# Performance work log

Hardware: AMD Instinct MI355X
Metric: run time of the kernel (lower is better)

Reference implementation:

```python
import jax, jax.numpy as jnp
import numpy as np

D_MODEL = 1024
D_INNER = 2048   # d_model * expansion_factor(2)
D_CONV = 4
N_EXPERTS = 8
TOP_K = 2


def setup_inputs() -> dict:
    key = jax.random.key(0)
    ks = jax.random.split(key, 6)
    s = 0.02
    return {
        "x": jax.random.normal(ks[0], (4, 2048, D_MODEL), jnp.float32),
        "Wr": jax.random.normal(ks[1], (N_EXPERTS, D_MODEL), jnp.float32) * s,
        "br": jnp.zeros((N_EXPERTS,), jnp.float32),
        "Win": jax.random.normal(ks[2], (N_EXPERTS, 2 * D_INNER, D_MODEL), jnp.float32) * s,
        "conv_w": jax.random.normal(ks[3], (N_EXPERTS, D_INNER, D_CONV), jnp.float32) * s,
        "conv_b": jnp.zeros((N_EXPERTS, D_INNER), jnp.float32),
        "Dp": jnp.ones((N_EXPERTS, D_INNER), jnp.float32),
        "Wout": jax.random.normal(ks[4], (N_EXPERTS, D_MODEL, D_INNER), jnp.float32) * s,
    }


def reference(x, Wr, br, Win, conv_w, conv_b, Dp, Wout):
    B, L, C = x.shape
    xf = x.reshape(-1, C)                                   # [N, C]
    logits = xf @ Wr.T + br                                 # [N, E]
    probs = jax.nn.softmax(logits.astype(jnp.float32), axis=-1)
    tw, ti = jax.lax.top_k(probs, TOP_K)                    # [N, k]
    tw = tw / jnp.sum(tw, axis=-1, keepdims=True)
    oh = jax.nn.one_hot(ti, N_EXPERTS, dtype=jnp.float32)   # [N, k, E]
    load = oh.sum(1).mean(0)                                # [E]
    aux_loss = jnp.sum(load * load)
    # per-token combine weight for each expert (sum over top-k slots)
    cw = jnp.einsum('nk,nke->ne', tw, oh)                   # [N, E]
    out = jnp.zeros_like(xf)
    for j in range(N_EXPERTS):
        # Per-token expert (L=1 inside the original loop): causal depthwise
        # conv with left padding reduces to last-tap * x + bias.
        xz = xf @ Win[j].T                                  # [N, 2*D_INNER]
        xi, z = xz[:, :D_INNER], xz[:, D_INNER:]
        xa = jax.nn.silu(xi * conv_w[j, :, -1] + conv_b[j])
        y = xa * Dp[j] * jax.nn.silu(z)
        out = out + cw[:, j:j + 1].astype(xf.dtype) * (y @ Wout[j].T)
    return out.reshape(B, L, C), aux_loss
```

## Files before the change

### kernel.cpp

```cpp
#include <hip/hip_runtime.h>
#include <hip/hip_bf16.h>
#include <stdint.h>

#define NTOK 8192
#define CDIM 1024
#define DIN  2048
#define NEXP 8
#define NSLOT (NTOK * 2)

typedef __bf16 bf16x8 __attribute__((ext_vector_type(8)));
typedef float  f32x4  __attribute__((ext_vector_type(4)));

typedef __attribute__((address_space(1))) const unsigned char GBUF;
typedef __attribute__((address_space(3))) unsigned char LBUF;

__device__ __forceinline__ void gload_lds16(const void* g, void* l) {
    __builtin_amdgcn_global_load_lds((GBUF*)g, (LBUF*)l, 16, 0, 0);
}

__device__ __forceinline__ ushort f2bf(float f) {
    union { float f; unsigned u; } v; v.f = f;
    unsigned u = v.u;
    u += 0x7fffu + ((u >> 16) & 1u);
    return (ushort)(u >> 16);
}
__device__ __forceinline__ float bf2f(ushort u) {
    union { float f; unsigned u; } v; v.u = ((unsigned)u) << 16; return v.f;
}
__device__ __forceinline__ float silu_f(float x) { return x / (1.f + __expf(-x)); }

__device__ __forceinline__ bf16x8 lds_swz(const ushort* L, int row, int kof) {
    return *(const bf16x8*)&L[row * 64 + ((((kof >> 3) ^ row) & 7) << 3)];
}

#define WAITV(N) asm volatile("s_waitcnt vmcnt(" #N ")" ::: "memory")
#define BARR     __builtin_amdgcn_s_barrier()

__global__ void __launch_bounds__(256) k_cvt(const float* __restrict__ src,
                                             ushort* __restrict__ dst, int n4) {
    int i = blockIdx.x * 256 + threadIdx.x;
    int stride = gridDim.x * 256;
    for (; i < n4; i += stride) {
        float4 v = ((const float4*)src)[i];
        ushort4 o;
        o.x = f2bf(v.x); o.y = f2bf(v.y); o.z = f2bf(v.z); o.w = f2bf(v.w);
        ((ushort4*)dst)[i] = o;
    }
}

__global__ void __launch_bounds__(256) k_router(
    const float* __restrict__ x, const float* __restrict__ Wr,
    const float* __restrict__ br, int* __restrict__ counts,
    int* __restrict__ tok_e, float* __restrict__ tok_w,
    ushort* __restrict__ xb) {
    int wave = blockIdx.x * 4 + (threadIdx.x >> 6);
    int lane = threadIdx.x & 63;
    const float4* row = (const float4*)(x + (size_t)wave * CDIM);
    ushort4* xrow = (ushort4*)(xb + (size_t)wave * CDIM);
    float acc[NEXP];
#pragma unroll
    for (int e = 0; e < NEXP; ++e) acc[e] = 0.f;
#pragma unroll
    for (int j = 0; j < 4; ++j) {
        float4 v = row[j * 64 + lane];
        ushort4 o;
        o.x = f2bf(v.x); o.y = f2bf(v.y); o.z = f2bf(v.z); o.w = f2bf(v.w);
        xrow[j * 64 + lane] = o;
#pragma unroll
        for (int e = 0; e < NEXP; ++e) {
            float4 w = ((const float4*)(Wr + e * CDIM))[j * 64 + lane];
            acc[e] += v.x * w.x + v.y * w.y + v.z * w.z + v.w * w.w;
        }
    }
#pragma unroll
    for (int off = 32; off > 0; off >>= 1)
#pragma unroll
        for (int e = 0; e < NEXP; ++e) acc[e] += __shfl_xor(acc[e], off, 64);
    if (lane == 0) {
        float l[NEXP];
#pragma unroll
        for (int e = 0; e < NEXP; ++e) l[e] = acc[e] + br[e];
        int i0 = 0; float l0 = l[0];
#pragma unroll
        for (int e = 1; e < NEXP; ++e) if (l[e] > l0) { l0 = l[e]; i0 = e; }
        int i1 = -1; float l1 = -1e30f;
#pragma unroll
        for (int e = 0; e < NEXP; ++e) if (e != i0 && l[e] > l1) { l1 = l[e]; i1 = e; }
        float s  = __expf(l1 - l0);
        float w0 = 1.f / (1.f + s);
        float w1 = 1.f - w0;
        tok_e[wave * 2] = i0; tok_e[wave * 2 + 1] = i1;
        tok_w[wave * 2] = w0; tok_w[wave * 2 + 1] = w1;
        atomicAdd(&counts[i0], 1); atomicAdd(&counts[i1], 1);
    }
}

__global__ void k_scan(const int* __restrict__ counts, int* __restrict__ offsets,
                       float* __restrict__ out_aux) {
    if (threadIdx.x == 0 && blockIdx.x == 0) {
        int o = 0;
        for (int e = 0; e < NEXP; ++e) { offsets[e] = o; o += counts[e]; }
        offsets[NEXP] = o;
        float aux = 0.f;
        for (int e = 0; e < NEXP; ++e) {
            float ld = (float)counts[e] * (1.f / (float)NTOK);
            aux += ld * ld;
        }
        *out_aux = aux;
    }
}

__global__ void __launch_bounds__(256) k_scatter(
    const int* __restrict__ tok_e, const float* __restrict__ tok_w,
    const int* __restrict__ offsets, int* __restrict__ cursor,
    int* __restrict__ perm_token, int* __restrict__ tok_slot) {
    int t = blockIdx.x * 256 + threadIdx.x;
    if (t >= NTOK) return;
#pragma unroll
    for (int k = 0; k < 2; ++k) {
        int e = tok_e[t * 2 + k];
        int pos = atomicAdd(&cursor[e], 1);
        int s = offsets[e] + pos;
        perm_token[s] = t;
        tok_slot[t * 2 + k] = s;
    }
}

__global__ void __launch_bounds__(512, 2) k_gemm1(
    const ushort* __restrict__ xb, const ushort* __restrict__ Winb,
    const float* __restrict__ conv_w, const float* __restrict__ conv_b,
    const float* __restrict__ Dp, const int* __restrict__ counts,
    const int* __restrict__ offsets, const int* __restrict__ perm_token,
    ushort* __restrict__ y) {
    int h = blockIdx.x;
    int vb = (h & 7) * 160 + (h >> 3);
    int e   = vb / 160;
    int r   = vb % 160;
    int mt0 = r >> 4;
    int nt  = r & 15;
    int cnt = counts[e];
    if (cnt == 0) return;
    int base = offsets[e];
    int mtiles = (cnt + 255) >> 8;
    int n0 = nt * 128;

    __shared__ ushort aL[2][256 * 64];
    __shared__ ushort bL[2][256 * 64];

    int tid = threadIdx.x, lane = tid & 63, w = tid >> 6;
    int Mw = w >> 1, Nw = w & 1;
    const ushort* WinE = Winb + (size_t)e * (2 * DIN) * CDIM;
    int schunk = ((tid & 7) ^ ((tid >> 3) & 7)) << 3;

    uint bsrc[4];
#pragma unroll
    for (int i = 0; i < 4; ++i) {
        int rr = i * 64 + (tid >> 3);
        int grow = (rr < 128) ? (n0 + rr) : (DIN + n0 + (rr - 128));
        bsrc[i] = (uint)grow * CDIM + schunk;
    }

    for (int mt = mt0; mt < mtiles; mt += 10) {
        int rem = cnt - mt * 256;
        uint asrc[4];
#pragma unroll
        for (int i = 0; i < 4; ++i) {
            int rr = i * 64 + (tid >> 3);
            int sidx = base + mt * 256 + (rr < rem ? rr : 0);
            asrc[i] = (uint)perm_token[sidx] * CDIM + schunk;
        }

        f32x4 accXi[4][4], accZ[4][4];
#pragma unroll
        for (int m = 0; m < 4; ++m)
#pragma unroll
            for (int n = 0; n < 4; ++n) {
                accXi[m][n] = f32x4{0.f, 0.f, 0.f, 0.f};
                accZ[m][n]  = f32x4{0.f, 0.f, 0.f, 0.f};
            }

        auto stgA = [&](int bi, int ko, int i, int j) {
            gload_lds16(xb + asrc[i] + ko, &aL[bi][(i * 512 + tid) * 8]);
            gload_lds16(xb + asrc[j] + ko, &aL[bi][(j * 512 + tid) * 8]);
        };
        auto stgB = [&](int bi, int ko, int i, int j) {
            gload_lds16(WinE + bsrc[i] + ko, &bL[bi][(i * 512 + tid) * 8]);
            gload_lds16(WinE + bsrc[j] + ko, &bL[bi][(j * 512 + tid) * 8]);
        };

        bf16x8 af0[4], af1[4], bx[4], bz[4];
        stgA(0, 0, 0, 1); stgA(0, 0, 2, 3); stgB(0, 0, 0, 1); stgB(0, 0, 2, 3);

#pragma unroll 1
        for (int kt = 0; kt < 16; ++kt) {
            int cur = kt & 1, nxt = cur ^ 1;
            const ushort* A = aL[cur];
            const ushort* B = bL[cur];
            int ko = (kt + 1) * 64;
            bool st = kt < 15;
            WAITV(2);
            BARR;
#pragma unroll
            for (int m = 0; m < 4; ++m)
                af0[m] = lds_swz(A, Mw * 64 + m * 16 + (lane & 15), (lane >> 4) * 8);
#pragma unroll
            for (int n = 0; n < 4; ++n)
                bx[n] = lds_swz(B, Nw * 64 + n * 16 + (lane & 15), (lane >> 4) * 8);
            if (st) stgA(nxt, ko, 0, 1);
            __builtin_amdgcn_s_setprio(1);
#pragma unroll
            for (int m = 0; m < 4; ++m)
#pragma unroll
                for (int n = 0; n < 4; ++n)
                    accXi[m][n] = __builtin_amdgcn_mfma_f32_16x16x32_bf16(af0[m], bx[n], accXi[m][n], 0, 0, 0);
            __builtin_amdgcn_s_setprio(0);
            if (st) { WAITV(2); } else { WAITV(0); }
            BARR;
#pragma unroll
            for (int n = 0; n < 4; ++n)
                bz[n] = lds_swz(B, 128 + Nw * 64 + n * 16 + (lane & 15), (lane >> 4) * 8);
            if (st) stgA(nxt, ko, 2, 3);
            __builtin_amdgcn_s_setprio(1);
#pragma unroll
            for (int m = 0; m < 4; ++m)
#pragma unroll
                for (int n = 0; n < 4; ++n)
                    accZ[m][n] = __builtin_amdgcn_mfma_f32_16x16x32_bf16(af0[m], bz[n], accZ[m][n], 0, 0, 0);
            __builtin_amdgcn_s_setprio(0);
            BARR;
#pragma unroll
            for (int m = 0; m < 4; ++m)
                af1[m] = lds_swz(A, Mw * 64 + m * 16 + (lane & 15), 32 + (lane >> 4) * 8);
#pragma unroll
            for (int n = 0; n < 4; ++n)
                bx[n] = lds_swz(B, Nw * 64 + n * 16 + (lane & 15), 32 + (lane >> 4) * 8);
            if (st) stgB(nxt, ko, 0, 1);
            __builtin_amdgcn_s_setprio(1);
#pragma unroll
            for (int m = 0; m < 4; ++m)
#pragma unroll
                for (int n = 0; n < 4; ++n)
                    accXi[m][n] = __builtin_amdgcn_mfma_f32_16x16x32_bf16(af1[m], bx[n], accXi[m][n], 0, 0, 0);
            __builtin_amdgcn_s_setprio(0);
            BARR;
#pragma unroll
            for (int n = 0; n < 4; ++n)
                bz[n] = lds_swz(B, 128 + Nw * 64 + n * 16 + (lane & 15), 32 + (lane >> 4) * 8);
            if (st) stgB(nxt, ko, 2, 3);
            __builtin_amdgcn_s_setprio(1);
#pragma unroll
            for (int m = 0; m < 4; ++m)
#pragma unroll
                for (int n = 0; n < 4; ++n)
                    accZ[m][n] = __builtin_amdgcn_mfma_f32_16x16x32_bf16(af1[m], bz[n], accZ[m][n], 0, 0, 0);
            __builtin_amdgcn_s_setprio(0);
        }
        __syncthreads();

#pragma unroll
        for (int n = 0; n < 4; ++n) {
            int c = n0 + Nw * 64 + n * 16 + (lane & 15);
            float cwl = conv_w[((size_t)e * DIN + c) * 4 + 3];
            float cb  = conv_b[(size_t)e * DIN + c];
            float dp  = Dp[(size_t)e * DIN + c];
#pragma unroll
            for (int m = 0; m < 4; ++m)
#pragma unroll
                for (int q = 0; q < 4; ++q) {
                    int rl = Mw * 64 + m * 16 + (lane >> 4) * 4 + q;
                    if (rl < rem) {
                        int slot = base + mt * 256 + rl;
                        float xi = accXi[m][n][q], z = accZ[m][n][q];
                        float yv = silu_f(xi * cwl + cb) * dp * silu_f(z);
                        y[(size_t)slot * DIN + c] = f2bf(yv);
                    }
                }
        }
        __syncthreads();
    }
}

__global__ void __launch_bounds__(512, 2) k_gemm2(
    const ushort* __restrict__ y, const ushort* __restrict__ Woutb,
    const int* __restrict__ counts, const int* __restrict__ offsets,
    ushort* __restrict__ so) {
    int h = blockIdx.x;
    int vb = (h & 7) * 32 + (h >> 3);
    int e   = vb >> 5;
    int r   = vb & 31;
    int nt  = r >> 3;
    int sp  = r & 7;
    int cnt = counts[e];
    if (cnt == 0) return;
    int base = offsets[e];
    int mtiles = (cnt + 255) >> 8;
    int c0 = nt * 256;

    __shared__ ushort aL[2][256 * 64];
    __shared__ ushort bL[2][256 * 64];

    int tid = threadIdx.x, lane = tid & 63, w = tid >> 6;
    int Mw = w >> 2, Nw = w & 3;
    const ushort* WoutE = Woutb + (size_t)e * CDIM * DIN;
    int schunk = ((tid & 7) ^ ((tid >> 3) & 7)) << 3;

    uint bsrc[4];
#pragma unroll
    for (int i = 0; i < 4; ++i) {
        int rr = i * 64 + (tid >> 3);
        bsrc[i] = (uint)(c0 + rr) * DIN + schunk;
    }

    for (int mt = sp; mt < mtiles; mt += 8) {
        int rem = cnt - mt * 256;
        uint asrc[4];
#pragma unroll
        for (int i = 0; i < 4; ++i) {
            int rr = i * 64 + (tid >> 3);
            int slot = base + mt * 256 + (rr < rem ? rr : 0);
            asrc[i] = (uint)slot * DIN + schunk;
        }
        f32x4 acc[8][4];
#pragma unroll
        for (int m = 0; m < 8; ++m)
#pragma unroll
            for (int n = 0; n < 4; ++n) acc[m][n] = f32x4{0.f, 0.f, 0.f, 0.f};

        auto stgA = [&](int bi, int ko, int i, int j) {
            gload_lds16(y + asrc[i] + ko, &aL[bi][(i * 512 + tid) * 8]);
            gload_lds16(y + asrc[j] + ko, &aL[bi][(j * 512 + tid) * 8]);
        };
        auto stgB = [&](int bi, int ko, int i, int j) {
            gload_lds16(WoutE + bsrc[i] + ko, &bL[bi][(i * 512 + tid) * 8]);
            gload_lds16(WoutE + bsrc[j] + ko, &bL[bi][(j * 512 + tid) * 8]);
        };

        bf16x8 afA[4], afB[4], bf0[4], bf1[4];
        stgA(0, 0, 0, 1); stgA(0, 0, 2, 3); stgB(0, 0, 0, 1); stgB(0, 0, 2, 3);

#pragma unroll 1
        for (int kt = 0; kt < 32; ++kt) {
            int cur = kt & 1, nxt = cur ^ 1;
            const ushort* A = aL[cur];
            const ushort* B = bL[cur];
            int ko = (kt + 1) * 64;
            bool st = kt < 31;
            WAITV(0);
            BARR;
#pragma unroll
            for (int m = 0; m < 4; ++m)
                afA[m] = lds_swz(A, Mw * 128 + m * 16 + (lane & 15), (lane >> 4) * 8);
#pragma unroll
            for (int n = 0; n < 4; ++n)
                bf0[n] = lds_swz(B, Nw * 64 + n * 16 + (lane & 15), (lane >> 4) * 8);
            if (st) stgA(nxt, ko, 0, 1);
            __builtin_amdgcn_s_setprio(1);
#pragma unroll
            for (int m = 0; m < 4; ++m)
#pragma unroll
                for (int n = 0; n < 4; ++n)
                    acc[m][n] = __builtin_amdgcn_mfma_f32_16x16x32_bf16(afA[m], bf0[n], acc[m][n], 0, 0, 0);
            __builtin_amdgcn_s_setprio(0);
            BARR;
#pragma unroll
            for (int m = 0; m < 4; ++m)
                afB[m] = lds_swz(A, Mw * 128 + 64 + m * 16 + (lane & 15), (lane >> 4) * 8);
            if (st) stgA(nxt, ko, 2, 3);
            __builtin_amdgcn_s_setprio(1);
#pragma unroll
            for (int m = 0; m < 4; ++m)
#pragma unroll
                for (int n = 0; n < 4; ++n)
                    acc[4 + m][n] = __builtin_amdgcn_mfma_f32_16x16x32_bf16(afB[m], bf0[n], acc[4 + m][n], 0, 0, 0);
            __builtin_amdgcn_s_setprio(0);
            BARR;
#pragma unroll
            for (int m = 0; m < 4; ++m)
                afA[m] = lds_swz(A, Mw * 128 + m * 16 + (lane & 15), 32 + (lane >> 4) * 8);
#pragma unroll
            for (int n = 0; n < 4; ++n)
                bf1[n] = lds_swz(B, Nw * 64 + n * 16 + (lane & 15), 32 + (lane >> 4) * 8);
            if (st) stgB(nxt, ko, 0, 1);
            __builtin_amdgcn_s_setprio(1);
#pragma unroll
            for (int m = 0; m < 4; ++m)
#pragma unroll
                for (int n = 0; n < 4; ++n)
                    acc[m][n] = __builtin_amdgcn_mfma_f32_16x16x32_bf16(afA[m], bf1[n], acc[m][n], 0, 0, 0);
            __builtin_amdgcn_s_setprio(0);
            BARR;
#pragma unroll
            for (int m = 0; m < 4; ++m)
                afB[m] = lds_swz(A, Mw * 128 + 64 + m * 16 + (lane & 15), 32 + (lane >> 4) * 8);
            if (st) stgB(nxt, ko, 2, 3);
            __builtin_amdgcn_s_setprio(1);
#pragma unroll
            for (int m = 0; m < 4; ++m)
#pragma unroll
                for (int n = 0; n < 4; ++n)
                    acc[4 + m][n] = __builtin_amdgcn_mfma_f32_16x16x32_bf16(afB[m], bf1[n], acc[4 + m][n], 0, 0, 0);
            __builtin_amdgcn_s_setprio(0);
        }
        __syncthreads();

#pragma unroll
        for (int m = 0; m < 8; ++m)
#pragma unroll
            for (int q = 0; q < 4; ++q) {
                int rl = Mw * 128 + m * 16 + (lane >> 4) * 4 + q;
                if (rl < rem) {
                    int slot = base + mt * 256 + rl;
#pragma unroll
                    for (int n = 0; n < 4; ++n) {
                        int col = c0 + Nw * 64 + n * 16 + (lane & 15);
                        so[(size_t)slot * CDIM + col] = f2bf(acc[m][n][q]);
                    }
                }
            }
        __syncthreads();
    }
}

__global__ void __launch_bounds__(256) k_combine(
    const ushort* __restrict__ so, const int* __restrict__ tok_slot,
    const float* __restrict__ tok_w, float* __restrict__ out) {
    int i = blockIdx.x * 256 + threadIdx.x;
    int t  = i >> 7;
    int c8 = (i & 127) << 3;
    int s0 = tok_slot[t * 2], s1 = tok_slot[t * 2 + 1];
    float w0 = tok_w[t * 2],  w1 = tok_w[t * 2 + 1];
    uint4 a = *(const uint4*)(so + (size_t)s0 * CDIM + c8);
    uint4 b = *(const uint4*)(so + (size_t)s1 * CDIM + c8);
    const ushort* au = (const ushort*)&a;
    const ushort* bu = (const ushort*)&b;
    float4 o0, o1;
    o0.x = w0 * bf2f(au[0]) + w1 * bf2f(bu[0]);
    o0.y = w0 * bf2f(au[1]) + w1 * bf2f(bu[1]);
    o0.z = w0 * bf2f(au[2]) + w1 * bf2f(bu[2]);
    o0.w = w0 * bf2f(au[3]) + w1 * bf2f(bu[3]);
    o1.x = w0 * bf2f(au[4]) + w1 * bf2f(bu[4]);
    o1.y = w0 * bf2f(au[5]) + w1 * bf2f(bu[5]);
    o1.z = w0 * bf2f(au[6]) + w1 * bf2f(bu[6]);
    o1.w = w0 * bf2f(au[7]) + w1 * bf2f(bu[7]);
    float4* dst = (float4*)(out + (size_t)t * CDIM + c8);
    dst[0] = o0; dst[1] = o1;
}

extern "C" void kernel_launch(void* const* d_in, const int* in_sizes, int n_in,
                              void* d_out, int out_size, void* d_ws, size_t ws_size,
                              hipStream_t stream) {
    const float* x      = (const float*)d_in[0];
    const float* Wr     = (const float*)d_in[1];
    const float* br     = (const float*)d_in[2];
    const float* Win    = (const float*)d_in[3];
    const float* conv_w = (const float*)d_in[4];
    const float* conv_b = (const float*)d_in[5];
    const float* Dp     = (const float*)d_in[6];
    const float* Wout   = (const float*)d_in[7];
    float* out = (float*)d_out;

    char* ws = (char*)d_ws;
    int*    counts     = (int*)(ws + 0);
    int*    offsets    = (int*)(ws + 64);
    int*    cursor     = (int*)(ws + 128);
    int*    tok_e      = (int*)(ws + 4096);
    float*  tok_w      = (float*)(ws + 4096 + 1 * 65536);
    int*    perm_token = (int*)(ws + 4096 + 2 * 65536);
    int*    tok_slot   = (int*)(ws + 4096 + 3 * 65536);
    const size_t MB = 1u << 20;
    ushort* y     = (ushort*)(ws + MB);
    ushort* xb    = (ushort*)(ws + MB + 67108864);
    ushort* winb  = (ushort*)(ws + MB + 67108864 + 16777216);
    ushort* woutb = (ushort*)(ws + MB + 67108864 + 16777216 + 67108864);
    ushort* so    = winb;

    hipMemsetAsync(ws, 0, 256, stream);

    k_cvt<<<2048, 256, 0, stream>>>(Win,  winb,  NEXP * 2 * DIN * CDIM / 4);
    k_cvt<<<1024, 256, 0, stream>>>(Wout, woutb, NEXP * CDIM * DIN / 4);

    k_router<<<NTOK / 4, 256, 0, stream>>>(x, Wr, br, counts, tok_e, tok_w, xb);
    k_scan<<<1, 64, 0, stream>>>(counts, offsets, out + (size_t)NTOK * CDIM);
    k_scatter<<<NTOK / 256, 256, 0, stream>>>(tok_e, tok_w, offsets, cursor, perm_token, tok_slot);

    k_gemm1<<<NEXP * 160, 512, 0, stream>>>(xb, winb, conv_w, conv_b, Dp,
                                            counts, offsets, perm_token, y);
    k_gemm2<<<NEXP * 32, 512, 0, stream>>>(y, woutb, counts, offsets, so);
    k_combine<<<NTOK * 128 / 256, 256, 0, stream>>>(so, tok_slot, tok_w, out);
}
```

Measured before the change: 626.3 us.

## Flatten gemm2 into global tile list with smaller tiles and fuse weight conversions

The scan now computes per-expert tile prefix offsets, and gemm2 switches from a fixed 8-expert by 32-block grid to a flat persistent loop over all (expert, m-tile, n-tile) work items. Tiles shrink to 256x128 with a single LDS buffer and a simple load/sync/compute loop, and launch bounds rise to allow more resident blocks. This is meant to fix load imbalance across experts and under-filled CUs. The cost is losing the double-buffered, prefetch-interleaved pipeline, so global loads are no longer overlapped with MFMA within a block. The two fp32-to-bf16 weight conversion launches are also merged into one kernel.

```diff
diff --git a/kernel.cpp b/kernel.cpp
--- a/kernel.cpp
+++ b/kernel.cpp
@@ -36,15 +36,20 @@
 #define WAITV(N) asm volatile("s_waitcnt vmcnt(" #N ")" ::: "memory")
 #define BARR     __builtin_amdgcn_s_barrier()
 
-__global__ void __launch_bounds__(256) k_cvt(const float* __restrict__ src,
-                                             ushort* __restrict__ dst, int n4) {
+__global__ void __launch_bounds__(256) k_cvt2(
+    const float* __restrict__ srcA, ushort* __restrict__ dstA, int nA4,
+    const float* __restrict__ srcB, ushort* __restrict__ dstB, int nB4) {
     int i = blockIdx.x * 256 + threadIdx.x;
     int stride = gridDim.x * 256;
-    for (; i < n4; i += stride) {
-        float4 v = ((const float4*)src)[i];
+    int ntot = nA4 + nB4;
+    for (; i < ntot; i += stride) {
+        const float4* s; ushort4* d; int j;
+        if (i < nA4) { s = (const float4*)srcA; d = (ushort4*)dstA; j = i; }
+        else         { s = (const float4*)srcB; d = (ushort4*)dstB; j = i - nA4; }
+        float4 v = s[j];
         ushort4 o;
         o.x = f2bf(v.x); o.y = f2bf(v.y); o.z = f2bf(v.z); o.w = f2bf(v.w);
-        ((ushort4*)dst)[i] = o;
+        d[j] = o;
     }
 }
 
@@ -96,11 +101,17 @@
 }
 
 __global__ void k_scan(const int* __restrict__ counts, int* __restrict__ offsets,
-                       float* __restrict__ out_aux) {
+                       int* __restrict__ tileoff, float* __restrict__ out_aux) {
     if (threadIdx.x == 0 && blockIdx.x == 0) {
-        int o = 0;
-        for (int e = 0; e < NEXP; ++e) { offsets[e] = o; o += counts[e]; }
+        int o = 0, tp = 0;
+        for (int e = 0; e < NEXP; ++e) {
+            offsets[e] = o;
+            tileoff[e] = tp;
+            o += counts[e];
+            tp += (counts[e] + 255) >> 8;
+        }
         offsets[NEXP] = o;
+        tileoff[NEXP] = tp;
         float aux = 0.f;
         for (int e = 0; e < NEXP; ++e) {
             float ld = (float)counts[e] * (1.f / (float)NTOK);
@@ -280,134 +291,87 @@
     }
 }
 
-__global__ void __launch_bounds__(512, 2) k_gemm2(
+__global__ void __launch_bounds__(512, 6) k_gemm2(
     const ushort* __restrict__ y, const ushort* __restrict__ Woutb,
     const int* __restrict__ counts, const int* __restrict__ offsets,
-    ushort* __restrict__ so) {
-    int h = blockIdx.x;
-    int vb = (h & 7) * 32 + (h >> 3);
-    int e   = vb >> 5;
-    int r   = vb & 31;
-    int nt  = r >> 3;
-    int sp  = r & 7;
-    int cnt = counts[e];
-    if (cnt == 0) return;
-    int base = offsets[e];
-    int mtiles = (cnt + 255) >> 8;
-    int c0 = nt * 256;
-
-    __shared__ ushort aL[2][256 * 64];
-    __shared__ ushort bL[2][256 * 64];
+    const int* __restrict__ tileoff, ushort* __restrict__ so) {
+    __shared__ ushort aL[256 * 64];
+    __shared__ ushort bL[128 * 64];
 
     int tid = threadIdx.x, lane = tid & 63, w = tid >> 6;
-    int Mw = w >> 2, Nw = w & 3;
-    const ushort* WoutE = Woutb + (size_t)e * CDIM * DIN;
+    int Mw = w >> 1, Nw = w & 1;
     int schunk = ((tid & 7) ^ ((tid >> 3) & 7)) << 3;
 
-    uint bsrc[4];
-#pragma unroll
-    for (int i = 0; i < 4; ++i) {
-        int rr = i * 64 + (tid >> 3);
-        bsrc[i] = (uint)(c0 + rr) * DIN + schunk;
-    }
-
-    for (int mt = sp; mt < mtiles; mt += 8) {
+    int ntiles = tileoff[NEXP] * 8;
+    int b = blockIdx.x;
+    int virt = (b & 7) * 96 + (b >> 3);
+
+    for (int t = virt; t < ntiles; t += 768) {
+        int pair = t >> 3, nt = t & 7;
+        int e = 0;
+#pragma unroll
+        for (int k = 1; k < NEXP; ++k) if (pair >= tileoff[k]) e = k;
+        int mt = pair - tileoff[e];
+        int cnt = counts[e], base = offsets[e];
         int rem = cnt - mt * 256;
-        uint asrc[4];
+        int c0 = nt * 128;
+        const ushort* WoutE = Woutb + (size_t)e * CDIM * DIN;
+
+        uint asrc[4], bsrc[2];
 #pragma unroll
         for (int i = 0; i < 4; ++i) {
             int rr = i * 64 + (tid >> 3);
             int slot = base + mt * 256 + (rr < rem ? rr : 0);
             asrc[i] = (uint)slot * DIN + schunk;
         }
-        f32x4 acc[8][4];
-#pragma unroll
-        for (int m = 0; m < 8; ++m)
+#pragma unroll
+        for (int i = 0; i < 2; ++i) {
+            int rr = i * 64 + (tid >> 3);
+            bsrc[i] = (uint)(c0 + rr) * DIN + schunk;
+        }
+
+        f32x4 acc[4][4];
+#pragma unroll
+        for (int m = 0; m < 4; ++m)
 #pragma unroll
             for (int n = 0; n < 4; ++n) acc[m][n] = f32x4{0.f, 0.f, 0.f, 0.f};
-
-        auto stgA = [&](int bi, int ko, int i, int j) {
-            gload_lds16(y + asrc[i] + ko, &aL[bi][(i * 512 + tid) * 8]);
-            gload_lds16(y + asrc[j] + ko, &aL[bi][(j * 512 + tid) * 8]);
-        };
-        auto stgB = [&](int bi, int ko, int i, int j) {
-            gload_lds16(WoutE + bsrc[i] + ko, &bL[bi][(i * 512 + tid) * 8]);
-            gload_lds16(WoutE + bsrc[j] + ko, &bL[bi][(j * 512 + tid) * 8]);
-        };
-
-        bf16x8 afA[4], afB[4], bf0[4], bf1[4];
-        stgA(0, 0, 0, 1); stgA(0, 0, 2, 3); stgB(0, 0, 0, 1); stgB(0, 0, 2, 3);
 
 #pragma unroll 1
         for (int kt = 0; kt < 32; ++kt) {
-            int cur = kt & 1, nxt = cur ^ 1;
-            const ushort* A = aL[cur];
-            const ushort* B = bL[cur];
-            int ko = (kt + 1) * 64;
-            bool st = kt < 31;
-            WAITV(0);
-            BARR;
-#pragma unroll
-            for (int m = 0; m < 4; ++m)
-                afA[m] = lds_swz(A, Mw * 128 + m * 16 + (lane & 15), (lane >> 4) * 8);
-#pragma unroll
-            for (int n = 0; n < 4; ++n)
-                bf0[n] = lds_swz(B, Nw * 64 + n * 16 + (lane & 15), (lane >> 4) * 8);
-            if (st) stgA(nxt, ko, 0, 1);
-            __builtin_amdgcn_s_setprio(1);
-#pragma unroll
-            for (int m = 0; m < 4; ++m)
+            int ko = kt * 64;
+            gload_lds16(y + asrc[0] + ko, &aL[(0 * 512 + tid) * 8]);
+            gload_lds16(y + asrc[1] + ko, &aL[(1 * 512 + tid) * 8]);
+            gload_lds16(y + asrc[2] + ko, &aL[(2 * 512 + tid) * 8]);
+            gload_lds16(y + asrc[3] + ko, &aL[(3 * 512 + tid) * 8]);
+            gload_lds16(WoutE + bsrc[0] + ko, &bL[(0 * 512 + tid) * 8]);
+            gload_lds16(WoutE + bsrc[1] + ko, &bL[(1 * 512 + tid) * 8]);
+            __syncthreads();
+#pragma unroll
+            for (int kk = 0; kk < 64; kk += 32) {
+                int kof = kk + (lane >> 4) * 8;
+                bf16x8 af[4], bf[4];
+#pragma unroll
+                for (int m = 0; m < 4; ++m)
+                    af[m] = lds_swz(aL, Mw * 64 + m * 16 + (lane & 15), kof);
 #pragma unroll
                 for (int n = 0; n < 4; ++n)
-                    acc[m][n] = __builtin_amdgcn_mfma_f32_16x16x32_bf16(afA[m], bf0[n], acc[m][n], 0, 0, 0);
-            __builtin_amdgcn_s_setprio(0);
-            BARR;
-#pragma unroll
-            for (int m = 0; m < 4; ++m)
-                afB[m] = lds_swz(A, Mw * 128 + 64 + m * 16 + (lane & 15), (lane >> 4) * 8);
-            if (st) stgA(nxt, ko, 2, 3);
-            __builtin_amdgcn_s_setprio(1);
-#pragma unroll
-            for (int m = 0; m < 4; ++m)
-#pragma unroll
-                for (int n = 0; n < 4; ++n)
-                    acc[4 + m][n] = __builtin_amdgcn_mfma_f32_16x16x32_bf16(afB[m], bf0[n], acc[4 + m][n], 0, 0, 0);
-            __builtin_amdgcn_s_setprio(0);
-            BARR;
-#pragma unroll
-            for (int m = 0; m < 4; ++m)
-                afA[m] = lds_swz(A, Mw * 128 + m * 16 + (lane & 15), 32 + (lane >> 4) * 8);
-#pragma unroll
-            for (int n = 0; n < 4; ++n)
-                bf1[n] = lds_swz(B, Nw * 64 + n * 16 + (lane & 15), 32 + (lane >> 4) * 8);
-            if (st) stgB(nxt, ko, 0, 1);
-            __builtin_amdgcn_s_setprio(1);
-#pragma unroll
-            for (int m = 0; m < 4; ++m)
-#pragma unroll
-                for (int n = 0; n < 4; ++n)
-                    acc[m][n] = __builtin_amdgcn_mfma_f32_16x16x32_bf16(afA[m], bf1[n], acc[m][n], 0, 0, 0);
-            __builtin_amdgcn_s_setprio(0);
-            BARR;
-#pragma unroll
-            for (int m = 0; m < 4; ++m)
-                afB[m] = lds_swz(A, Mw * 128 + 64 + m * 16 + (lane & 15), 32 + (lane >> 4) * 8);
-            if (st) stgB(nxt, ko, 2, 3);
-            __builtin_amdgcn_s_setprio(1);
-#pragma unroll
-            for (int m = 0; m < 4; ++m)
-#pragma unroll
-                for (int n = 0; n < 4; ++n)
-                    acc[4 + m][n] = __builtin_amdgcn_mfma_f32_16x16x32_bf16(afB[m], bf1[n], acc[4 + m][n], 0, 0, 0);
-            __builtin_amdgcn_s_setprio(0);
-        }
-        __syncthreads();
-
-#pragma unroll
-        for (int m = 0; m < 8; ++m)
+                    bf[n] = lds_swz(bL, Nw * 64 + n * 16 + (lane & 15), kof);
+                __builtin_amdgcn_s_setprio(1);
+#pragma unroll
+                for (int m = 0; m < 4; ++m)
+#pragma unroll
+                    for (int n = 0; n < 4; ++n)
+                        acc[m][n] = __builtin_amdgcn_mfma_f32_16x16x32_bf16(af[m], bf[n], acc[m][n], 0, 0, 0);
+                __builtin_amdgcn_s_setprio(0);
+            }
+            __syncthreads();
+        }
+
+#pragma unroll
+        for (int m = 0; m < 4; ++m)
 #pragma unroll
             for (int q = 0; q < 4; ++q) {
-                int rl = Mw * 128 + m * 16 + (lane >> 4) * 4 + q;
+                int rl = Mw * 64 + m * 16 + (lane >> 4) * 4 + q;
                 if (rl < rem) {
                     int slot = base + mt * 256 + rl;
 #pragma unroll
@@ -417,7 +381,6 @@
                     }
                 }
             }
-        __syncthreads();
     }
 }
 
@@ -463,6 +426,7 @@
     int*    counts     = (int*)(ws + 0);
     int*    offsets    = (int*)(ws + 64);
     int*    cursor     = (int*)(ws + 128);
+    int*    tileoff    = (int*)(ws + 192);
     int*    tok_e      = (int*)(ws + 4096);
     float*  tok_w      = (float*)(ws + 4096 + 1 * 65536);
     int*    perm_token = (int*)(ws + 4096 + 2 * 65536);
@@ -476,15 +440,15 @@
 
     hipMemsetAsync(ws, 0, 256, stream);
 
-    k_cvt<<<2048, 256, 0, stream>>>(Win,  winb,  NEXP * 2 * DIN * CDIM / 4);
-    k_cvt<<<1024, 256, 0, stream>>>(Wout, woutb, NEXP * CDIM * DIN / 4);
+    k_cvt2<<<3072, 256, 0, stream>>>(Win,  winb,  NEXP * 2 * DIN * CDIM / 4,
+                                     Wout, woutb, NEXP * CDIM * DIN / 4);
 
     k_router<<<NTOK / 4, 256, 0, stream>>>(x, Wr, br, counts, tok_e, tok_w, xb);
-    k_scan<<<1, 64, 0, stream>>>(counts, offsets, out + (size_t)NTOK * CDIM);
+    k_scan<<<1, 64, 0, stream>>>(counts, offsets, tileoff, out + (size_t)NTOK * CDIM);
     k_scatter<<<NTOK / 256, 256, 0, stream>>>(tok_e, tok_w, offsets, cursor, perm_token, tok_slot);
 
     k_gemm1<<<NEXP * 160, 512, 0, stream>>>(xb, winb, conv_w, conv_b, Dp,
                                             counts, offsets, perm_token, y);
-    k_gemm2<<<NEXP * 32, 512, 0, stream>>>(y, woutb, counts, offsets, so);
+    k_gemm2<<<768, 512, 0, stream>>>(y, woutb, counts, offsets, tileoff, so);
     k_combine<<<NTOK * 128 / 256, 256, 0, stream>>>(so, tok_slot, tok_w, out);
 }
```

New measurement: 1.333 ms. 113% more time.
